# Kernel optimization log

Hardware: AMD Instinct MI355X
Metric: run time of the kernel (lower is better)

Reference implementation:

```python
import jax, jax.numpy as jnp
import numpy as np

E, TWO_I, H = 8, 3072, 2048
I = TWO_I // 2
T = 16384

def setup_inputs() -> dict:
    key = jax.random.key(0)
    k1, k2, k3 = jax.random.split(key, 3)
    scale_gu = 1.0 / np.sqrt(H)
    scale_dn = 1.0 / np.sqrt(I)
    return {
        "current_state": jax.random.normal(k1, (T, H), dtype=jnp.float32),
        "gate_up_proj": jax.random.normal(k2, (E, TWO_I, H), dtype=jnp.float32) * scale_gu,
        "down_proj": jax.random.normal(k3, (E, H, I), dtype=jnp.float32) * scale_dn,
        "expert_idx": 3,
    }

def reference(current_state, gate_up_proj, down_proj, expert_idx):
    # F.linear(x, W) == x @ W.T
    w_gu = gate_up_proj[expert_idx]            # [2I, H]
    w_dn = down_proj[expert_idx]               # [H, I]
    gu = jnp.einsum("th,ih->ti", current_state, w_gu)  # [T, 2I]
    gate, up = jnp.split(gu, 2, axis=-1)       # each [T, I]
    hidden = jax.nn.silu(gate) * up            # SwiGLU gating
    return jnp.einsum("ti,hi->th", hidden, w_dn)  # [T, H]
```

## Files before the change

### kernel.cpp

```cpp
#include <hip/hip_runtime.h>
#include <hip/hip_bf16.h>


namespace {

constexpr int T_ = 16384;
constexpr int H_ = 2048;
constexpr int I_ = 1536;

typedef short short8 __attribute__((ext_vector_type(8)));
typedef float f32x4 __attribute__((ext_vector_type(4)));
typedef unsigned short ushort4v __attribute__((ext_vector_type(4)));

__device__ __forceinline__ unsigned short f2bf(float f) {
    union { float f; unsigned u; } v; v.f = f;
    return (unsigned short)((v.u + 0x7FFFu + ((v.u >> 16) & 1u)) >> 16);
}

typedef __attribute__((address_space(1))) const void gvoid;
typedef __attribute__((address_space(3))) void lvoid;
__device__ __forceinline__ void gload16(const void* g, void* l) {
    __builtin_amdgcn_global_load_lds((gvoid*)g, (lvoid*)l, 16, 0, 0);
}

__global__ void k_cvt(const float* __restrict__ base, const int* __restrict__ eidx,
                      long sliceElems, unsigned short* __restrict__ dst, int n4) {
    const float* src = base + (size_t)(*eidx) * (size_t)sliceElems;
    int i = blockIdx.x * blockDim.x + threadIdx.x;
    const int stride = gridDim.x * blockDim.x;
    for (; i < n4; i += stride) {
        f32x4 v = ((const f32x4*)src)[i];
        ushort4v h = { f2bf(v[0]), f2bf(v[1]), f2bf(v[2]), f2bf(v[3]) };
        ((ushort4v*)dst)[i] = h;
    }
}

__global__ __launch_bounds__(256, 2) void k_gemm1_swiglu(
    const unsigned short* __restrict__ xb, const unsigned short* __restrict__ wgub,
    unsigned short* __restrict__ hidden)
{
    __shared__ unsigned short lds[3 * 128 * 64];
    unsigned short* ldsA  = lds;
    unsigned short* ldsBg = lds + 128 * 64;
    unsigned short* ldsBu = lds + 2 * 128 * 64;

    const int tid  = threadIdx.x;
    const int lane = tid & 63;
    const int wv   = tid >> 6;
    const int wr   = wv >> 1, wc = wv & 1;

    const int nb = (blockIdx.x & 7) * 192 + (blockIdx.x >> 3);
    const int bx = nb % 12, by = nb / 12;
    const int m0 = by * 128;
    const int n0 = bx * 128;

    f32x4 accG[4][4], accU[4][4];
    #pragma unroll
    for (int a = 0; a < 4; ++a)
        #pragma unroll
        for (int b = 0; b < 4; ++b) { accG[a][b] = (f32x4)0.0f; accU[a][b] = (f32x4)0.0f; }

    const int drow = lane >> 3;
    const int gcol = (((lane & 7) ^ drow) * 8);
    const int l15 = lane & 15;
    const int l4  = lane >> 4;
    const int sw  = l15 & 7;

    for (int k0 = 0; k0 < H_; k0 += 64) {
        __syncthreads();
        #pragma unroll
        for (int r = 0; r < 4; ++r) {
            const int row  = r * 32 + wv * 8 + drow;
            const int loff = r * 2048 + wv * 512;
            gload16(xb   + (size_t)(m0 + row)      * H_ + k0 + gcol, ldsA  + loff);
            gload16(wgub + (size_t)(n0 + row)      * H_ + k0 + gcol, ldsBg + loff);
            gload16(wgub + (size_t)(I_ + n0 + row) * H_ + k0 + gcol, ldsBu + loff);
        }
        __syncthreads();

        #pragma unroll
        for (int kk = 0; kk < 2; ++kk) {
            const int sl = ((kk * 4 + l4) ^ sw) * 8;
            short8 af[4], bg[4], bu[4];
            #pragma unroll
            for (int a = 0; a < 4; ++a) {
                const int r = wr * 64 + a * 16 + l15;
                af[a] = *(const short8*)(ldsA + r * 64 + sl);
            }
            #pragma unroll
            for (int b = 0; b < 4; ++b) {
                const int r = wc * 64 + b * 16 + l15;
                bg[b] = *(const short8*)(ldsBg + r * 64 + sl);
                bu[b] = *(const short8*)(ldsBu + r * 64 + sl);
            }
            #pragma unroll
            for (int a = 0; a < 4; ++a)
                #pragma unroll
                for (int b = 0; b < 4; ++b) {
                    accG[a][b] = __builtin_amdgcn_mfma_f32_16x16x32_bf16(af[a], bg[b], accG[a][b], 0, 0, 0);
                    accU[a][b] = __builtin_amdgcn_mfma_f32_16x16x32_bf16(af[a], bu[b], accU[a][b], 0, 0, 0);
                }
        }
    }

    #pragma unroll
    for (int a = 0; a < 4; ++a)
        #pragma unroll
        for (int b = 0; b < 4; ++b)
            #pragma unroll
            for (int j = 0; j < 4; ++j) {
                const int row = m0 + wr * 64 + a * 16 + l4 * 4 + j;
                const int col = n0 + wc * 64 + b * 16 + l15;
                const float g = accG[a][b][j];
                const float u = accU[a][b][j];
                const float s = g / (1.0f + __expf(-g));
                hidden[(size_t)row * I_ + col] = f2bf(s * u);
            }
}

__global__ __launch_bounds__(256, 2) void k_gemm2(
    const unsigned short* __restrict__ hidden, const unsigned short* __restrict__ wdnb,
    float* __restrict__ out)
{
    __shared__ unsigned short lds[2 * 128 * 64];
    unsigned short* ldsA = lds;
    unsigned short* ldsB = lds + 128 * 64;

    const int tid  = threadIdx.x;
    const int lane = tid & 63;
    const int wv   = tid >> 6;
    const int wr   = wv >> 1, wc = wv & 1;

    const int nb = (blockIdx.x & 7) * 256 + (blockIdx.x >> 3);
    const int bx = nb % 16, by = nb / 16;
    const int m0 = by * 128;
    const int n0 = bx * 128;

    f32x4 acc[4][4];
    #pragma unroll
    for (int a = 0; a < 4; ++a)
        #pragma unroll
        for (int b = 0; b < 4; ++b) acc[a][b] = (f32x4)0.0f;

    const int drow = lane >> 3;
    const int gcol = (((lane & 7) ^ drow) * 8);
    const int l15 = lane & 15;
    const int l4  = lane >> 4;
    const int sw  = l15 & 7;

    for (int k0 = 0; k0 < I_; k0 += 64) {
        __syncthreads();
        #pragma unroll
        for (int r = 0; r < 4; ++r) {
            const int row  = r * 32 + wv * 8 + drow;
            const int loff = r * 2048 + wv * 512;
            gload16(hidden + (size_t)(m0 + row) * I_ + k0 + gcol, ldsA + loff);
            gload16(wdnb   + (size_t)(n0 + row) * I_ + k0 + gcol, ldsB + loff);
        }
        __syncthreads();

        #pragma unroll
        for (int kk = 0; kk < 2; ++kk) {
            const int sl = ((kk * 4 + l4) ^ sw) * 8;
            short8 af[4], bw[4];
            #pragma unroll
            for (int a = 0; a < 4; ++a) {
                const int r = wr * 64 + a * 16 + l15;
                af[a] = *(const short8*)(ldsA + r * 64 + sl);
            }
            #pragma unroll
            for (int b = 0; b < 4; ++b) {
                const int r = wc * 64 + b * 16 + l15;
                bw[b] = *(const short8*)(ldsB + r * 64 + sl);
            }
            #pragma unroll
            for (int a = 0; a < 4; ++a)
                #pragma unroll
                for (int b = 0; b < 4; ++b)
                    acc[a][b] = __builtin_amdgcn_mfma_f32_16x16x32_bf16(af[a], bw[b], acc[a][b], 0, 0, 0);
        }
    }

    #pragma unroll
    for (int a = 0; a < 4; ++a)
        #pragma unroll
        for (int b = 0; b < 4; ++b)
            #pragma unroll
            for (int j = 0; j < 4; ++j) {
                const int row = m0 + wr * 64 + a * 16 + l4 * 4 + j;
                const int col = n0 + wc * 64 + b * 16 + l15;
                out[(size_t)row * H_ + col] = acc[a][b][j];
            }
}

}

extern "C" void kernel_launch(void* const* d_in, const int* in_sizes, int n_in,
                              void* d_out, int out_size, void* d_ws, size_t ws_size,
                              hipStream_t stream) {
    const float* x   = (const float*)d_in[0];
    const float* wgu = (const float*)d_in[1];
    const float* wdn = (const float*)d_in[2];
    const int* eidx  = (const int*)d_in[3];
    float* out = (float*)d_out;

    unsigned short* xb     = (unsigned short*)d_out;
    unsigned short* hidden = (unsigned short*)d_ws;
    unsigned short* wgub   = (unsigned short*)((char*)d_ws + 50331648);
    unsigned short* wdnb   = (unsigned short*)((char*)d_ws + 62914560);

    k_cvt<<<2048, 256, 0, stream>>>(x, eidx, 0L, xb, (T_ * H_) / 4);
    k_cvt<<<2048, 256, 0, stream>>>(wgu, eidx, (long)(2 * I_) * H_, wgub, (2 * I_ * H_) / 4);
    k_cvt<<<2048, 256, 0, stream>>>(wdn, eidx, (long)H_ * I_, wdnb, (H_ * I_) / 4);
    k_gemm1_swiglu<<<dim3((I_ / 128) * (T_ / 128)), 256, 0, stream>>>(xb, wgub, hidden);
    k_gemm2<<<dim3((H_ / 128) * (T_ / 128)), 256, 0, stream>>>(hidden, wdnb, out);
}
```

Baseline: 338.4 us.

## Load A operand directly into registers and merge conversion kernels

Both GEMM kernels now load the activation (A) fragments straight from global memory into registers instead of staging them through LDS. Only the weight tiles still go through LDS, which cuts LDS traffic and shared memory per block. The three conversion launches are also merged into one kernel to save launch overhead. In exchange, the direct A loads are 16-byte per-lane accesses with a row stride, so coalescing is worse. Each A row is also now fetched separately by both wave columns (wc) instead of once per block, and the loads are not prefetched ahead of the compute.

```diff
diff --git a/kernel.cpp b/kernel.cpp
--- a/kernel.cpp
+++ b/kernel.cpp
@@ -23,15 +23,26 @@
     __builtin_amdgcn_global_load_lds((gvoid*)g, (lvoid*)l, 16, 0, 0);
 }
 
-__global__ void k_cvt(const float* __restrict__ base, const int* __restrict__ eidx,
-                      long sliceElems, unsigned short* __restrict__ dst, int n4) {
-    const float* src = base + (size_t)(*eidx) * (size_t)sliceElems;
-    int i = blockIdx.x * blockDim.x + threadIdx.x;
+__global__ void k_cvt_all(const float* __restrict__ x, const float* __restrict__ wgu,
+                          const float* __restrict__ wdn, const int* __restrict__ eidx,
+                          unsigned short* __restrict__ xb, unsigned short* __restrict__ wgub,
+                          unsigned short* __restrict__ wdnb) {
+    const int e = *eidx;
+    const int n1 = T_ * H_ / 4;
+    const int n2 = 2 * I_ * H_ / 4;
+    const int n3 = H_ * I_ / 4;
+    const int ntot = n1 + n2 + n3;
+    const float* wgu_e = wgu + (size_t)e * (size_t)(2 * I_) * H_;
+    const float* wdn_e = wdn + (size_t)e * (size_t)H_ * I_;
     const int stride = gridDim.x * blockDim.x;
-    for (; i < n4; i += stride) {
-        f32x4 v = ((const f32x4*)src)[i];
+    for (int i = blockIdx.x * blockDim.x + threadIdx.x; i < ntot; i += stride) {
+        const float* src; unsigned short* dst; int j;
+        if (i < n1)           { src = x;     dst = xb;   j = i; }
+        else if (i < n1 + n2) { src = wgu_e; dst = wgub; j = i - n1; }
+        else                  { src = wdn_e; dst = wdnb; j = i - n1 - n2; }
+        f32x4 v = ((const f32x4*)src)[j];
         ushort4v h = { f2bf(v[0]), f2bf(v[1]), f2bf(v[2]), f2bf(v[3]) };
-        ((ushort4v*)dst)[i] = h;
+        ((ushort4v*)dst)[j] = h;
     }
 }
 
@@ -39,10 +50,9 @@
     const unsigned short* __restrict__ xb, const unsigned short* __restrict__ wgub,
     unsigned short* __restrict__ hidden)
 {
-    __shared__ unsigned short lds[3 * 128 * 64];
-    unsigned short* ldsA  = lds;
-    unsigned short* ldsBg = lds + 128 * 64;
-    unsigned short* ldsBu = lds + 2 * 128 * 64;
+    __shared__ unsigned short lds[2 * 128 * 64];
+    unsigned short* ldsBg = lds;
+    unsigned short* ldsBu = lds + 128 * 64;
 
     const int tid  = threadIdx.x;
     const int lane = tid & 63;
@@ -66,13 +76,20 @@
     const int l4  = lane >> 4;
     const int sw  = l15 & 7;
 
+    const unsigned short* aBase = xb + (size_t)(m0 + wr * 64 + l15) * H_ + l4 * 8;
+
     for (int k0 = 0; k0 < H_; k0 += 64) {
         __syncthreads();
+        short8 af[2][4];
+        #pragma unroll
+        for (int kk = 0; kk < 2; ++kk)
+            #pragma unroll
+            for (int a = 0; a < 4; ++a)
+                af[kk][a] = *(const short8*)(aBase + (size_t)(a * 16) * H_ + k0 + kk * 32);
         #pragma unroll
         for (int r = 0; r < 4; ++r) {
             const int row  = r * 32 + wv * 8 + drow;
             const int loff = r * 2048 + wv * 512;
-            gload16(xb   + (size_t)(m0 + row)      * H_ + k0 + gcol, ldsA  + loff);
             gload16(wgub + (size_t)(n0 + row)      * H_ + k0 + gcol, ldsBg + loff);
             gload16(wgub + (size_t)(I_ + n0 + row) * H_ + k0 + gcol, ldsBu + loff);
         }
@@ -81,12 +98,7 @@
         #pragma unroll
         for (int kk = 0; kk < 2; ++kk) {
             const int sl = ((kk * 4 + l4) ^ sw) * 8;
-            short8 af[4], bg[4], bu[4];
-            #pragma unroll
-            for (int a = 0; a < 4; ++a) {
-                const int r = wr * 64 + a * 16 + l15;
-                af[a] = *(const short8*)(ldsA + r * 64 + sl);
-            }
+            short8 bg[4], bu[4];
             #pragma unroll
             for (int b = 0; b < 4; ++b) {
                 const int r = wc * 64 + b * 16 + l15;
@@ -97,8 +109,8 @@
             for (int a = 0; a < 4; ++a)
                 #pragma unroll
                 for (int b = 0; b < 4; ++b) {
-                    accG[a][b] = __builtin_amdgcn_mfma_f32_16x16x32_bf16(af[a], bg[b], accG[a][b], 0, 0, 0);
-                    accU[a][b] = __builtin_amdgcn_mfma_f32_16x16x32_bf16(af[a], bu[b], accU[a][b], 0, 0, 0);
+                    accG[a][b] = __builtin_amdgcn_mfma_f32_16x16x32_bf16(af[kk][a], bg[b], accG[a][b], 0, 0, 0);
+                    accU[a][b] = __builtin_amdgcn_mfma_f32_16x16x32_bf16(af[kk][a], bu[b], accU[a][b], 0, 0, 0);
                 }
         }
     }
@@ -122,9 +134,7 @@
     const unsigned short* __restrict__ hidden, const unsigned short* __restrict__ wdnb,
     float* __restrict__ out)
 {
-    __shared__ unsigned short lds[2 * 128 * 64];
-    unsigned short* ldsA = lds;
-    unsigned short* ldsB = lds + 128 * 64;
+    __shared__ unsigned short lds[128 * 64];
 
     const int tid  = threadIdx.x;
     const int lane = tid & 63;
@@ -148,36 +158,38 @@
     const int l4  = lane >> 4;
     const int sw  = l15 & 7;
 
+    const unsigned short* aBase = hidden + (size_t)(m0 + wr * 64 + l15) * I_ + l4 * 8;
+
     for (int k0 = 0; k0 < I_; k0 += 64) {
         __syncthreads();
+        short8 af[2][4];
+        #pragma unroll
+        for (int kk = 0; kk < 2; ++kk)
+            #pragma unroll
+            for (int a = 0; a < 4; ++a)
+                af[kk][a] = *(const short8*)(aBase + (size_t)(a * 16) * I_ + k0 + kk * 32);
         #pragma unroll
         for (int r = 0; r < 4; ++r) {
             const int row  = r * 32 + wv * 8 + drow;
             const int loff = r * 2048 + wv * 512;
-            gload16(hidden + (size_t)(m0 + row) * I_ + k0 + gcol, ldsA + loff);
-            gload16(wdnb   + (size_t)(n0 + row) * I_ + k0 + gcol, ldsB + loff);
+            gload16(wdnb + (size_t)(n0 + row) * I_ + k0 + gcol, lds + loff);
         }
         __syncthreads();
 
         #pragma unroll
         for (int kk = 0; kk < 2; ++kk) {
             const int sl = ((kk * 4 + l4) ^ sw) * 8;
-            short8 af[4], bw[4];
-            #pragma unroll
-            for (int a = 0; a < 4; ++a) {
-                const int r = wr * 64 + a * 16 + l15;
-                af[a] = *(const short8*)(ldsA + r * 64 + sl);
-            }
+            short8 bw[4];
             #pragma unroll
             for (int b = 0; b < 4; ++b) {
                 const int r = wc * 64 + b * 16 + l15;
-                bw[b] = *(const short8*)(ldsB + r * 64 + sl);
+                bw[b] = *(const short8*)(lds + r * 64 + sl);
             }
             #pragma unroll
             for (int a = 0; a < 4; ++a)
                 #pragma unroll
                 for (int b = 0; b < 4; ++b)
-                    acc[a][b] = __builtin_amdgcn_mfma_f32_16x16x32_bf16(af[a], bw[b], acc[a][b], 0, 0, 0);
+                    acc[a][b] = __builtin_amdgcn_mfma_f32_16x16x32_bf16(af[kk][a], bw[b], acc[a][b], 0, 0, 0);
         }
     }
 
@@ -209,9 +221,7 @@
     unsigned short* wgub   = (unsigned short*)((char*)d_ws + 50331648);
     unsigned short* wdnb   = (unsigned short*)((char*)d_ws + 62914560);
 
-    k_cvt<<<2048, 256, 0, stream>>>(x, eidx, 0L, xb, (T_ * H_) / 4);
-    k_cvt<<<2048, 256, 0, stream>>>(wgu, eidx, (long)(2 * I_) * H_, wgub, (2 * I_ * H_) / 4);
-    k_cvt<<<2048, 256, 0, stream>>>(wdn, eidx, (long)H_ * I_, wdnb, (H_ * I_) / 4);
+    k_cvt_all<<<2048, 256, 0, stream>>>(x, wgu, wdn, eidx, xb, wgub, wdnb);
     k_gemm1_swiglu<<<dim3((I_ / 128) * (T_ / 128)), 256, 0, stream>>>(xb, wgub, hidden);
     k_gemm2<<<dim3((H_ / 128) * (T_ / 128)), 256, 0, stream>>>(hidden, wdnb, out);
 }
```

After: 498.5 us. +47.3%, slower.

## Double-buffer LDS in down-projection GEMM and merge conversion kernels

Applied to the files above, without the earlier changes.

The second GEMM now uses two LDS buffers, so the global-to-LDS load of the next K tile is issued before the MFMA work on the current tile, with one vmcnt wait and barrier per iteration instead of two syncthreads. The three fp32-to-bf16 conversion launches are merged into one kernel that dispatches by index range, saving two launches. The LDS footprint of gemm2 doubles to 64 KB per block, which may limit occupancy, and the merged conversion adds branching per element.

```diff
diff --git a/kernel.cpp b/kernel.cpp
--- a/kernel.cpp
+++ b/kernel.cpp
@@ -23,15 +23,29 @@
     __builtin_amdgcn_global_load_lds((gvoid*)g, (lvoid*)l, 16, 0, 0);
 }
 
-__global__ void k_cvt(const float* __restrict__ base, const int* __restrict__ eidx,
-                      long sliceElems, unsigned short* __restrict__ dst, int n4) {
-    const float* src = base + (size_t)(*eidx) * (size_t)sliceElems;
-    int i = blockIdx.x * blockDim.x + threadIdx.x;
+#define SBAR() do { __builtin_amdgcn_s_barrier(); __builtin_amdgcn_sched_barrier(0); } while (0)
+#define VMCNT0() do { asm volatile("s_waitcnt vmcnt(0)" ::: "memory"); __builtin_amdgcn_sched_barrier(0); } while (0)
+
+__global__ void k_cvt_all(const float* __restrict__ x, const float* __restrict__ wgu,
+                          const float* __restrict__ wdn, const int* __restrict__ eidx,
+                          unsigned short* __restrict__ xb, unsigned short* __restrict__ wgub,
+                          unsigned short* __restrict__ wdnb) {
+    const int e = *eidx;
+    const int n1 = T_ * H_ / 4;
+    const int n2 = 2 * I_ * H_ / 4;
+    const int n3 = H_ * I_ / 4;
+    const int ntot = n1 + n2 + n3;
+    const float* wgu_e = wgu + (size_t)e * (size_t)(2 * I_) * H_;
+    const float* wdn_e = wdn + (size_t)e * (size_t)H_ * I_;
     const int stride = gridDim.x * blockDim.x;
-    for (; i < n4; i += stride) {
-        f32x4 v = ((const f32x4*)src)[i];
+    for (int i = blockIdx.x * blockDim.x + threadIdx.x; i < ntot; i += stride) {
+        const float* src; unsigned short* dst; int j;
+        if (i < n1)           { src = x;     dst = xb;   j = i; }
+        else if (i < n1 + n2) { src = wgu_e; dst = wgub; j = i - n1; }
+        else                  { src = wdn_e; dst = wdnb; j = i - n1 - n2; }
+        f32x4 v = ((const f32x4*)src)[j];
         ushort4v h = { f2bf(v[0]), f2bf(v[1]), f2bf(v[2]), f2bf(v[3]) };
-        ((ushort4v*)dst)[i] = h;
+        ((ushort4v*)dst)[j] = h;
     }
 }
 
@@ -122,9 +136,7 @@
     const unsigned short* __restrict__ hidden, const unsigned short* __restrict__ wdnb,
     float* __restrict__ out)
 {
-    __shared__ unsigned short lds[2 * 128 * 64];
-    unsigned short* ldsA = lds;
-    unsigned short* ldsB = lds + 128 * 64;
+    __shared__ unsigned short lds[2 * 2 * 128 * 64];
 
     const int tid  = threadIdx.x;
     const int lane = tid & 63;
@@ -148,17 +160,30 @@
     const int l4  = lane >> 4;
     const int sw  = l15 & 7;
 
-    for (int k0 = 0; k0 < I_; k0 += 64) {
-        __syncthreads();
+    constexpr int NT = I_ / 64;
+
+    auto stage = [&](int t) {
+        unsigned short* dA = lds + (t & 1) * 16384;
+        unsigned short* dB = dA + 8192;
+        const int kS = t * 64;
         #pragma unroll
         for (int r = 0; r < 4; ++r) {
             const int row  = r * 32 + wv * 8 + drow;
             const int loff = r * 2048 + wv * 512;
-            gload16(hidden + (size_t)(m0 + row) * I_ + k0 + gcol, ldsA + loff);
-            gload16(wdnb   + (size_t)(n0 + row) * I_ + k0 + gcol, ldsB + loff);
-        }
-        __syncthreads();
-
+            gload16(hidden + (size_t)(m0 + row) * I_ + kS + gcol, dA + loff);
+            gload16(wdnb   + (size_t)(n0 + row) * I_ + kS + gcol, dB + loff);
+        }
+    };
+
+    stage(0);
+    VMCNT0();
+    SBAR();
+
+    for (int t = 0; t < NT; ++t) {
+        if (t + 1 < NT) stage(t + 1);
+
+        const unsigned short* bA = lds + (t & 1) * 16384;
+        const unsigned short* bB = bA + 8192;
         #pragma unroll
         for (int kk = 0; kk < 2; ++kk) {
             const int sl = ((kk * 4 + l4) ^ sw) * 8;
@@ -166,12 +191,12 @@
             #pragma unroll
             for (int a = 0; a < 4; ++a) {
                 const int r = wr * 64 + a * 16 + l15;
-                af[a] = *(const short8*)(ldsA + r * 64 + sl);
+                af[a] = *(const short8*)(bA + r * 64 + sl);
             }
             #pragma unroll
             for (int b = 0; b < 4; ++b) {
                 const int r = wc * 64 + b * 16 + l15;
-                bw[b] = *(const short8*)(ldsB + r * 64 + sl);
+                bw[b] = *(const short8*)(bB + r * 64 + sl);
             }
             #pragma unroll
             for (int a = 0; a < 4; ++a)
@@ -179,6 +204,9 @@
                 for (int b = 0; b < 4; ++b)
                     acc[a][b] = __builtin_amdgcn_mfma_f32_16x16x32_bf16(af[a], bw[b], acc[a][b], 0, 0, 0);
         }
+
+        VMCNT0();
+        SBAR();
     }
 
     #pragma unroll
@@ -209,9 +237,7 @@
     unsigned short* wgub   = (unsigned short*)((char*)d_ws + 50331648);
     unsigned short* wdnb   = (unsigned short*)((char*)d_ws + 62914560);
 
-    k_cvt<<<2048, 256, 0, stream>>>(x, eidx, 0L, xb, (T_ * H_) / 4);
-    k_cvt<<<2048, 256, 0, stream>>>(wgu, eidx, (long)(2 * I_) * H_, wgub, (2 * I_ * H_) / 4);
-    k_cvt<<<2048, 256, 0, stream>>>(wdn, eidx, (long)H_ * I_, wdnb, (H_ * I_) / 4);
+    k_cvt_all<<<2048, 256, 0, stream>>>(x, wgu, wdn, eidx, xb, wgub, wdnb);
     k_gemm1_swiglu<<<dim3((I_ / 128) * (T_ / 128)), 256, 0, stream>>>(xb, wgub, hidden);
     k_gemm2<<<dim3((H_ / 128) * (T_ / 128)), 256, 0, stream>>>(hidden, wdnb, out);
 }
```

Result: no change. 337.4 us (-0.3%).
